# Kernel optimization log

Hardware: AMD Instinct MI355X
Metric: run time of the kernel (lower is better)

The kernel has to match this reference:

```python
import jax, jax.numpy as jnp
import numpy as np

S = 8192  # query length
T = 8192  # key/value length
D = 256   # head dim


def setup_inputs() -> dict:
    key = jax.random.key(0)
    kq, kk, kv = jax.random.split(key, 3)
    return {
        "query": jax.random.normal(kq, (S, D), dtype=jnp.float32),
        "key": jax.random.normal(kk, (T, D), dtype=jnp.float32),
        "value": jax.random.normal(kv, (T, D), dtype=jnp.float32),
    }


def reference(query, key, value):
    # attn_weights = Q @ K^T  (contract last dims, no batch dims)  -> [S, T]
    attn_weights = jnp.einsum("sd,td->st", query, key)
    # SoftmaxAttn: softmax over axes [ndim//2, ndim) == last axis for 2D
    attn_weights = jax.nn.softmax(attn_weights, axis=-1).astype(jnp.float32)
    # y = A @ V  -> [S, D]
    y = jnp.einsum("st,td->sd", attn_weights, value)
    return y
```

## Files before the change

### kernel.cpp

```cpp
#include <hip/hip_runtime.h>
#include <hip/hip_fp16.h>

#define S_LEN 8192
#define T_LEN 8192
#define D_DIM 256
#define QBLK 128
#define KVBLK 32
#define TSPLIT 8
#define NKV ((T_LEN / TSPLIT) / KVBLK)
#define NQT (S_LEN / QBLK)
#define KTILE_BYTES 16384
#define VTILE_BYTES 16384
#define RESCALE_THR 6.0f
#define LOG2E 1.44269504f

typedef _Float16 f16x8 __attribute__((ext_vector_type(8)));
typedef float f32x4 __attribute__((ext_vector_type(4)));

struct h4 { _Float16 h[4]; };

#define GLOAD_LDS16(g, l)                                              \
    __builtin_amdgcn_global_load_lds(                                  \
        (const __attribute__((address_space(1))) void*)(g),            \
        (__attribute__((address_space(3))) void*)(l), 16, 0, 0)

#define MFMA16(a, b, c) __builtin_amdgcn_mfma_f32_16x16x32_f16(a, b, c, 0, 0, 0)

#if __has_builtin(__builtin_amdgcn_exp2f)
#define EXP2(x) __builtin_amdgcn_exp2f(x)
#else
static __device__ __forceinline__ float EXP2(float x) {
    float y;
    asm("v_exp_f32 %0, %1" : "=v"(y) : "v"(x));
    return y;
}
#endif

__global__ __launch_bounds__(256) void cvt_kernel(const float* __restrict__ in,
                                                  _Float16* __restrict__ out, int n4) {
    int i = blockIdx.x * 256 + threadIdx.x;
    if (i < n4) {
        float4 v = ((const float4*)in)[i];
        h4 o;
        o.h[0] = (_Float16)(v.x * LOG2E); o.h[1] = (_Float16)(v.y * LOG2E);
        o.h[2] = (_Float16)(v.z * LOG2E); o.h[3] = (_Float16)(v.w * LOG2E);
        ((h4*)out)[i] = o;
    }
}

__global__ __launch_bounds__(256) void cvt_swz_kernel(const float* __restrict__ in,
                                                      _Float16* __restrict__ img,
                                                      int nchunks) {
    int id = blockIdx.x * 256 + threadIdx.x;
    if (id >= nchunks) return;
    int row = id >> 5, gr = id & 31;
    int t = row >> 5, r = row & 31;
    float4 a = *(const float4*)(in + (size_t)row * D_DIM + gr * 8);
    float4 b = *(const float4*)(in + (size_t)row * D_DIM + gr * 8 + 4);
    f16x8 o;
    o[0] = (_Float16)a.x; o[1] = (_Float16)a.y; o[2] = (_Float16)a.z; o[3] = (_Float16)a.w;
    o[4] = (_Float16)b.x; o[5] = (_Float16)b.y; o[6] = (_Float16)b.z; o[7] = (_Float16)b.w;
    *(f16x8*)((char*)img + (size_t)t * KTILE_BYTES + (gr >> 2) * 2048 +
              ((r >> 4) << 10) + ((r & 15) << 6) + ((gr & 3) << 4)) = o;
}

__global__ __launch_bounds__(256) void vt_swz_kernel(const float* __restrict__ V,
                                                     _Float16* __restrict__ Vimg) {
    __shared__ float tile[32][260];
    const int t = blockIdx.x;
#pragma unroll
    for (int i = 0; i < 8; ++i) {
        int idx = i * 256 + threadIdx.x;
        int kr = idx >> 6, c4 = idx & 63;
        float4 v = *(const float4*)(V + ((size_t)t * 32 + kr) * D_DIM + c4 * 4);
        tile[kr][c4 * 4 + 0] = v.x;
        tile[kr][c4 * 4 + 1] = v.y;
        tile[kr][c4 * 4 + 2] = v.z;
        tile[kr][c4 * 4 + 3] = v.w;
    }
    __syncthreads();
#pragma unroll
    for (int i = 0; i < 4; ++i) {
        int gid = i * 256 + threadIdx.x;
        int d = gid >> 2, gk = gid & 3;
        f16x8 o;
#pragma unroll
        for (int j = 0; j < 8; ++j)
            o[j] = (_Float16)tile[(j >> 2) * 16 + gk * 4 + (j & 3)][d];
        *(f16x8*)((char*)Vimg + (size_t)t * VTILE_BYTES + ((d >> 4) << 10) +
                  (gk << 8) + ((d & 15) << 4)) = o;
    }
}

__global__ __launch_bounds__(256, 2) void attn_kernel(
    const _Float16* __restrict__ Qh, const _Float16* __restrict__ Kimg,
    const _Float16* __restrict__ Vimg, _Float16* __restrict__ Opart,
    float* __restrict__ ml) {
    __shared__ __align__(16) char smem[65536];
    const int tid = threadIdx.x;
    const int wave = tid >> 6, lane = tid & 63;
    const int g = lane >> 4, c = lane & 15;
    const int bid = blockIdx.x;
    const int qtile = bid >> 3, split = bid & 7;
    const int tile0 = split * NKV;
    const int rot = ((qtile >> 5) << 4) | ((qtile & 3) << 2);
    const int othr = tid * 16;
    const int kbase = ((lane & 15) << 6) | ((lane >> 4) << 4);
    const int vbase = lane << 4;

    f16x8 qf[2][8];
    {
        const size_t qrow0 = (size_t)qtile * QBLK + wave * 32 + c;
#pragma unroll
        for (int mi = 0; mi < 2; ++mi)
#pragma unroll
            for (int ks = 0; ks < 8; ++ks)
                qf[mi][ks] =
                    *(const f16x8*)(Qh + (qrow0 + mi * 16) * D_DIM + (ks * 4 + g) * 8);
    }
    asm volatile("s_waitcnt vmcnt(0)" ::: "memory");

    f32x4 acc[2][16];
#pragma unroll
    for (int mi = 0; mi < 2; ++mi)
#pragma unroll
        for (int dt = 0; dt < 16; ++dt) acc[mi][dt] = (f32x4){0.f, 0.f, 0.f, 0.f};
    float m[2] = {-1e30f, -1e30f};
    float l[2] = {0.f, 0.f};

    {
        const int t0 = tile0 + rot;
        const char* Kt = (const char*)Kimg + (size_t)t0 * KTILE_BYTES;
        const char* Vt = (const char*)Vimg + (size_t)t0 * VTILE_BYTES;
#pragma unroll
        for (int i = 0; i < 4; ++i) {
            GLOAD_LDS16(Kt + i * 4096 + othr, smem + i * 4096 + othr);
            GLOAD_LDS16(Vt + i * 4096 + othr, smem + 32768 + i * 4096 + othr);
        }
    }

    for (int kt = 0; kt < NKV; ++kt) {
        const int cur = kt & 1;
        if (kt + 1 < NKV) {
            const int tn = tile0 + ((kt + 1 + rot) & (NKV - 1));
            const char* Kt = (const char*)Kimg + (size_t)tn * KTILE_BYTES;
            const char* Vt = (const char*)Vimg + (size_t)tn * VTILE_BYTES;
            const int nb = (cur ^ 1) * 16384;
#pragma unroll
            for (int i = 0; i < 4; ++i) {
                GLOAD_LDS16(Kt + i * 4096 + othr, smem + nb + i * 4096 + othr);
                GLOAD_LDS16(Vt + i * 4096 + othr, smem + 32768 + nb + i * 4096 + othr);
            }
            asm volatile("s_waitcnt vmcnt(8)" ::: "memory");
        } else {
            asm volatile("s_waitcnt vmcnt(0)" ::: "memory");
        }
        __builtin_amdgcn_s_barrier();

        const char* sK = smem + cur * 16384;
        const char* sV = smem + 32768 + cur * 16384;

        f32x4 st[2][2];
#pragma unroll
        for (int mi = 0; mi < 2; ++mi)
#pragma unroll
            for (int ct = 0; ct < 2; ++ct) st[mi][ct] = (f32x4){0.f, 0.f, 0.f, 0.f};
        __builtin_amdgcn_s_setprio(1);
#pragma unroll
        for (int ks = 0; ks < 8; ++ks) {
            f16x8 kf0 = *(const f16x8*)(sK + ks * 2048 + kbase);
            f16x8 kf1 = *(const f16x8*)(sK + ks * 2048 + 1024 + kbase);
            st[0][0] = MFMA16(kf0, qf[0][ks], st[0][0]);
            st[0][1] = MFMA16(kf1, qf[0][ks], st[0][1]);
            st[1][0] = MFMA16(kf0, qf[1][ks], st[1][0]);
            st[1][1] = MFMA16(kf1, qf[1][ks], st[1][1]);
        }
        __builtin_amdgcn_s_setprio(0);

        union PU { unsigned int u[4]; f16x8 v; };
        PU pu[2];
#pragma unroll
        for (int mi = 0; mi < 2; ++mi) {
            float pm = fmaxf(fmaxf(fmaxf(st[mi][0][0], st[mi][0][1]),
                                   fmaxf(st[mi][0][2], st[mi][0][3])),
                             fmaxf(fmaxf(st[mi][1][0], st[mi][1][1]),
                                   fmaxf(st[mi][1][2], st[mi][1][3])));
            if (__any(pm > m[mi] + RESCALE_THR)) {
                pm = fmaxf(pm, __shfl_xor(pm, 16));
                pm = fmaxf(pm, __shfl_xor(pm, 32));
                float mn = fmaxf(m[mi], pm);
                float sc = EXP2(m[mi] - mn);
                m[mi] = mn;
                l[mi] *= sc;
                float fr[4];
#pragma unroll
                for (int r = 0; r < 4; ++r) fr[r] = __shfl(sc, (g << 4) | (g * 4 + r));
#pragma unroll
                for (int dt = 0; dt < 16; ++dt)
#pragma unroll
                    for (int r = 0; r < 4; ++r) acc[mi][dt][r] *= fr[r];
            }
            float rs = 0.f;
#pragma unroll
            for (int ct = 0; ct < 2; ++ct)
#pragma unroll
                for (int r = 0; r < 4; ++r) {
                    float p = EXP2(st[mi][ct][r] - m[mi]);
                    st[mi][ct][r] = p;
                    rs += p;
                }
            l[mi] += rs;
            pu[mi].u[0] = __builtin_bit_cast(
                unsigned int, __builtin_amdgcn_cvt_pkrtz(st[mi][0][0], st[mi][0][1]));
            pu[mi].u[1] = __builtin_bit_cast(
                unsigned int, __builtin_amdgcn_cvt_pkrtz(st[mi][0][2], st[mi][0][3]));
            pu[mi].u[2] = __builtin_bit_cast(
                unsigned int, __builtin_amdgcn_cvt_pkrtz(st[mi][1][0], st[mi][1][1]));
            pu[mi].u[3] = __builtin_bit_cast(
                unsigned int, __builtin_amdgcn_cvt_pkrtz(st[mi][1][2], st[mi][1][3]));
        }

        __builtin_amdgcn_s_setprio(1);
#pragma unroll
        for (int dt = 0; dt < 16; ++dt) {
            f16x8 vf = *(const f16x8*)(sV + dt * 1024 + vbase);
            acc[0][dt] = MFMA16(pu[0].v, vf, acc[0][dt]);
            acc[1][dt] = MFMA16(pu[1].v, vf, acc[1][dt]);
        }
        __builtin_amdgcn_s_setprio(0);

        __builtin_amdgcn_s_barrier();
    }

    _Float16* Ob = Opart + (size_t)(qtile * TSPLIT + split) * QBLK * D_DIM;
#pragma unroll
    for (int mi = 0; mi < 2; ++mi)
#pragma unroll
        for (int dt = 0; dt < 16; ++dt)
#pragma unroll
            for (int r = 0; r < 4; ++r) {
                int row = wave * 32 + mi * 16 + g * 4 + r;
                int col = dt * 16 + c;
                Ob[(size_t)row * D_DIM + col] = (_Float16)acc[mi][dt][r];
            }
#pragma unroll
    for (int mi = 0; mi < 2; ++mi) {
        l[mi] += __shfl_xor(l[mi], 16);
        l[mi] += __shfl_xor(l[mi], 32);
    }
    if (g == 0) {
        float* mlb = ml + (size_t)((qtile * TSPLIT + split) * QBLK) * 2;
#pragma unroll
        for (int mi = 0; mi < 2; ++mi) {
            int row = wave * 32 + mi * 16 + c;
            mlb[row * 2 + 0] = m[mi];
            mlb[row * 2 + 1] = l[mi];
        }
    }
}

__global__ __launch_bounds__(256) void combine_kernel(const _Float16* __restrict__ Opart,
                                                      const float* __restrict__ ml,
                                                      float* __restrict__ out) {
    int r = blockIdx.x;
    int qtile = r >> 7, rl = r & 127;
    int d = threadIdx.x;
    float mv[TSPLIT], lv[TSPLIT];
    float M = -1e30f;
#pragma unroll
    for (int s = 0; s < TSPLIT; ++s) {
        const float* mlb = ml + (size_t)((qtile * TSPLIT + s) * QBLK + rl) * 2;
        mv[s] = mlb[0];
        lv[s] = mlb[1];
        M = fmaxf(M, mv[s]);
    }
    float num = 0.f, den = 0.f;
#pragma unroll
    for (int s = 0; s < TSPLIT; ++s) {
        float w = EXP2(mv[s] - M);
        num += w * (float)Opart[((size_t)(qtile * TSPLIT + s) * QBLK + rl) * D_DIM + d];
        den += w * lv[s];
    }
    out[(size_t)r * D_DIM + d] = num / den;
}

extern "C" void kernel_launch(void* const* d_in, const int* in_sizes, int n_in,
                              void* d_out, int out_size, void* d_ws, size_t ws_size,
                              hipStream_t stream) {
    const float* Q = (const float*)d_in[0];
    const float* K = (const float*)d_in[1];
    const float* V = (const float*)d_in[2];
    float* out = (float*)d_out;
    char* ws = (char*)d_ws;

    _Float16* Qh = (_Float16*)ws;
    _Float16* Kimg = (_Float16*)(ws + (4 << 20));
    _Float16* Vimg = (_Float16*)(ws + (8 << 20));
    _Float16* Opart = (_Float16*)(ws + (12 << 20));
    float* ml = (float*)(ws + ((size_t)44 << 20));

    const int n4 = S_LEN * D_DIM / 4;
    const int nchunks = S_LEN * D_DIM / 8;
    cvt_kernel<<<n4 / 256, 256, 0, stream>>>(Q, Qh, n4);
    cvt_swz_kernel<<<nchunks / 256, 256, 0, stream>>>(K, Kimg, nchunks);
    vt_swz_kernel<<<T_LEN / 32, 256, 0, stream>>>(V, Vimg);

    attn_kernel<<<NQT * TSPLIT, 256, 0, stream>>>(Qh, Kimg, Vimg, Opart, ml);
    combine_kernel<<<S_LEN, 256, 0, stream>>>(Opart, ml, out);
}
```

Before: 105.0 us.

## Software-pipeline QK^T of the next KV tile with softmax and PV of the current

```diff
diff --git a/kernel.cpp b/kernel.cpp
--- a/kernel.cpp
+++ b/kernel.cpp
@@ -13,6 +13,7 @@
 #define VTILE_BYTES 16384
 #define RESCALE_THR 6.0f
 #define LOG2E 1.44269504f
+#define SMEM_BYTES 81920
 
 typedef _Float16 f16x8 __attribute__((ext_vector_type(8)));
 typedef float f32x4 __attribute__((ext_vector_type(4)));
@@ -96,7 +97,9 @@
     const _Float16* __restrict__ Qh, const _Float16* __restrict__ Kimg,
     const _Float16* __restrict__ Vimg, _Float16* __restrict__ Opart,
     float* __restrict__ ml) {
-    __shared__ __align__(16) char smem[65536];
+    extern __shared__ __align__(16) char smem[];
+    char* sK = smem;
+    char* sV = smem + 32768;
     const int tid = threadIdx.x;
     const int wave = tid >> 6, lane = tid & 63;
     const int g = lane >> 4, c = lane & 15;
@@ -108,6 +111,17 @@
     const int kbase = ((lane & 15) << 6) | ((lane >> 4) << 4);
     const int vbase = lane << 4;
 
+#define TILE_AT(k) (tile0 + (((k) + rot) & (NKV - 1)))
+#define STAGE_KV(k, kslot, vslot)                                                  \
+    {                                                                              \
+        const char* Kt = (const char*)Kimg + (size_t)TILE_AT(k) * KTILE_BYTES;     \
+        const char* Vt = (const char*)Vimg + (size_t)TILE_AT(k) * VTILE_BYTES;     \
+        _Pragma("unroll") for (int i = 0; i < 4; ++i) {                            \
+            GLOAD_LDS16(Kt + i * 4096 + othr, sK + (kslot)*16384 + i * 4096 + othr); \
+            GLOAD_LDS16(Vt + i * 4096 + othr, sV + (vslot)*16384 + i * 4096 + othr); \
+        }                                                                          \
+    }
+
     f16x8 qf[2][8];
     {
         const size_t qrow0 = (size_t)qtile * QBLK + wave * 32 + c;
@@ -128,54 +142,57 @@
     float m[2] = {-1e30f, -1e30f};
     float l[2] = {0.f, 0.f};
 
-    {
-        const int t0 = tile0 + rot;
-        const char* Kt = (const char*)Kimg + (size_t)t0 * KTILE_BYTES;
-        const char* Vt = (const char*)Vimg + (size_t)t0 * VTILE_BYTES;
-#pragma unroll
-        for (int i = 0; i < 4; ++i) {
-            GLOAD_LDS16(Kt + i * 4096 + othr, smem + i * 4096 + othr);
-            GLOAD_LDS16(Vt + i * 4096 + othr, smem + 32768 + i * 4096 + othr);
-        }
-    }
+    STAGE_KV(0, 0, 0);
+    STAGE_KV(1, 1, 1);
+    asm volatile("s_waitcnt vmcnt(8)" ::: "memory");
+    __builtin_amdgcn_s_barrier();
+
+    f32x4 st[2][2];
+#pragma unroll
+    for (int mi = 0; mi < 2; ++mi)
+#pragma unroll
+        for (int ct = 0; ct < 2; ++ct) st[mi][ct] = (f32x4){0.f, 0.f, 0.f, 0.f};
+    __builtin_amdgcn_s_setprio(1);
+#pragma unroll
+    for (int ks = 0; ks < 8; ++ks) {
+        f16x8 kf0 = *(const f16x8*)(sK + ks * 2048 + kbase);
+        f16x8 kf1 = *(const f16x8*)(sK + ks * 2048 + 1024 + kbase);
+        st[0][0] = MFMA16(kf0, qf[0][ks], st[0][0]);
+        st[0][1] = MFMA16(kf1, qf[0][ks], st[0][1]);
+        st[1][0] = MFMA16(kf0, qf[1][ks], st[1][0]);
+        st[1][1] = MFMA16(kf1, qf[1][ks], st[1][1]);
+    }
+    __builtin_amdgcn_s_setprio(0);
+    __builtin_amdgcn_s_barrier();
 
     for (int kt = 0; kt < NKV; ++kt) {
-        const int cur = kt & 1;
-        if (kt + 1 < NKV) {
-            const int tn = tile0 + ((kt + 1 + rot) & (NKV - 1));
-            const char* Kt = (const char*)Kimg + (size_t)tn * KTILE_BYTES;
-            const char* Vt = (const char*)Vimg + (size_t)tn * VTILE_BYTES;
-            const int nb = (cur ^ 1) * 16384;
-#pragma unroll
-            for (int i = 0; i < 4; ++i) {
-                GLOAD_LDS16(Kt + i * 4096 + othr, smem + nb + i * 4096 + othr);
-                GLOAD_LDS16(Vt + i * 4096 + othr, smem + 32768 + nb + i * 4096 + othr);
-            }
+        if (kt + 2 < NKV) {
+            STAGE_KV(kt + 2, kt & 1, (kt + 2) % 3);
             asm volatile("s_waitcnt vmcnt(8)" ::: "memory");
         } else {
             asm volatile("s_waitcnt vmcnt(0)" ::: "memory");
         }
         __builtin_amdgcn_s_barrier();
 
-        const char* sK = smem + cur * 16384;
-        const char* sV = smem + 32768 + cur * 16384;
-
-        f32x4 st[2][2];
+        f32x4 stn[2][2];
 #pragma unroll
         for (int mi = 0; mi < 2; ++mi)
 #pragma unroll
-            for (int ct = 0; ct < 2; ++ct) st[mi][ct] = (f32x4){0.f, 0.f, 0.f, 0.f};
-        __builtin_amdgcn_s_setprio(1);
-#pragma unroll
-        for (int ks = 0; ks < 8; ++ks) {
-            f16x8 kf0 = *(const f16x8*)(sK + ks * 2048 + kbase);
-            f16x8 kf1 = *(const f16x8*)(sK + ks * 2048 + 1024 + kbase);
-            st[0][0] = MFMA16(kf0, qf[0][ks], st[0][0]);
-            st[0][1] = MFMA16(kf1, qf[0][ks], st[0][1]);
-            st[1][0] = MFMA16(kf0, qf[1][ks], st[1][0]);
-            st[1][1] = MFMA16(kf1, qf[1][ks], st[1][1]);
-        }
-        __builtin_amdgcn_s_setprio(0);
+            for (int ct = 0; ct < 2; ++ct) stn[mi][ct] = (f32x4){0.f, 0.f, 0.f, 0.f};
+        if (kt + 1 < NKV) {
+            const char* sKb = sK + ((kt + 1) & 1) * 16384;
+            __builtin_amdgcn_s_setprio(1);
+#pragma unroll
+            for (int ks = 0; ks < 8; ++ks) {
+                f16x8 kf0 = *(const f16x8*)(sKb + ks * 2048 + kbase);
+                f16x8 kf1 = *(const f16x8*)(sKb + ks * 2048 + 1024 + kbase);
+                stn[0][0] = MFMA16(kf0, qf[0][ks], stn[0][0]);
+                stn[0][1] = MFMA16(kf1, qf[0][ks], stn[0][1]);
+                stn[1][0] = MFMA16(kf0, qf[1][ks], stn[1][0]);
+                stn[1][1] = MFMA16(kf1, qf[1][ks], stn[1][1]);
+            }
+            __builtin_amdgcn_s_setprio(0);
+        }
 
         union PU { unsigned int u[4]; f16x8 v; };
         PU pu[2];
@@ -220,14 +237,22 @@
                 unsigned int, __builtin_amdgcn_cvt_pkrtz(st[mi][1][2], st[mi][1][3]));
         }
 
-        __builtin_amdgcn_s_setprio(1);
-#pragma unroll
-        for (int dt = 0; dt < 16; ++dt) {
-            f16x8 vf = *(const f16x8*)(sV + dt * 1024 + vbase);
-            acc[0][dt] = MFMA16(pu[0].v, vf, acc[0][dt]);
-            acc[1][dt] = MFMA16(pu[1].v, vf, acc[1][dt]);
-        }
-        __builtin_amdgcn_s_setprio(0);
+        {
+            const char* sVb = sV + (kt % 3) * 16384;
+            __builtin_amdgcn_s_setprio(1);
+#pragma unroll
+            for (int dt = 0; dt < 16; ++dt) {
+                f16x8 vf = *(const f16x8*)(sVb + dt * 1024 + vbase);
+                acc[0][dt] = MFMA16(pu[0].v, vf, acc[0][dt]);
+                acc[1][dt] = MFMA16(pu[1].v, vf, acc[1][dt]);
+            }
+            __builtin_amdgcn_s_setprio(0);
+        }
+
+#pragma unroll
+        for (int mi = 0; mi < 2; ++mi)
+#pragma unroll
+            for (int ct = 0; ct < 2; ++ct) st[mi][ct] = stn[mi][ct];
 
         __builtin_amdgcn_s_barrier();
     }
@@ -305,6 +330,6 @@
     cvt_swz_kernel<<<nchunks / 256, 256, 0, stream>>>(K, Kimg, nchunks);
     vt_swz_kernel<<<T_LEN / 32, 256, 0, stream>>>(V, Vimg);
 
-    attn_kernel<<<NQT * TSPLIT, 256, 0, stream>>>(Qh, Kimg, Vimg, Opart, ml);
+    attn_kernel<<<NQT * TSPLIT, 256, SMEM_BYTES, stream>>>(Qh, Kimg, Vimg, Opart, ml);
     combine_kernel<<<S_LEN, 256, 0, stream>>>(Opart, ml, out);
 }
```

Result: slower. 107.6 us (+2.5%).
